# Optimization experiments

Measured on AMD Instinct MI355X. Metric: run time of the kernel, lower is better.

## Reference

```python
import jax, jax.numpy as jnp
import numpy as np

CURRENT_TIME = 1000.0
TIME_WEIGHT = 0.1
NEG_INF = -1e9


def setup_inputs() -> dict:
    key = jax.random.key(0)
    ks = jax.random.split(key, 7)
    B, M, D, C = 1024, 65536, 64, 16
    return {
        "query": jax.random.normal(ks[0], (B, D), dtype=jnp.float32),
        "context": jax.random.normal(ks[1], (B, C), dtype=jnp.float32),
        "mem_keys": jax.random.normal(ks[2], (M, D), dtype=jnp.float32) * 0.1,
        "mem_values": jax.random.normal(ks[3], (M, D), dtype=jnp.float32) * 0.1,
        "mem_contexts": jax.random.normal(ks[4], (M, C), dtype=jnp.float32) * 0.1,
        "mem_timestamps": jax.random.uniform(ks[5], (M, 1), dtype=jnp.float32) * CURRENT_TIME,
        "used_mask": jax.random.randint(ks[6], (M,), 0, 2) > 0,
    }


def reference(query, context, mem_keys, mem_values, mem_contexts, mem_timestamps, used_mask):
    # content score: [B, M]
    scores = jnp.einsum("bd,md->bm", query, mem_keys)
    # context score, scaled by 0.5
    scores = scores + 0.5 * jnp.einsum("bc,mc->bm", context, mem_contexts)
    # time-decay bias, scaled by 0.3 (broadcast over batch)
    decay = jnp.exp(-TIME_WEIGHT * (CURRENT_TIME - mem_timestamps[:, 0]))  # [M]
    scores = scores + 0.3 * decay[None, :]
    # unused slots get -1e9 exactly as torch.full init
    scores = jnp.where(used_mask[None, :], scores, NEG_INF)
    attn = jax.nn.softmax(scores, axis=-1)
    return jnp.einsum("bm,md->bd", attn, mem_values)
```

## Files before the change

kernel.cpp:

```cpp
#include <hip/hip_runtime.h>

typedef float f32x4 __attribute__((ext_vector_type(4)));
typedef __bf16 bf16x8 __attribute__((ext_vector_type(8)));
typedef unsigned int u32;
typedef unsigned short u16;

#define MTOT 65536
#define BTOT 1024
#define DD 64
#define LOG2E 1.44269504088896340736f
#define MFMA __builtin_amdgcn_mfma_f32_16x16x32_bf16

#define NROWBLK ((MTOT + BTOT) * 24 / 256)
#define NVTBLK  (MTOT / 64)
#define ESPACE  (DD * BTOT + BTOT)
#define NSLICE  8

__device__ __forceinline__ u16 f2bf(float f) { return __builtin_bit_cast(u16, (__bf16)f); }
__device__ __forceinline__ u32 pk2(float a, float b) {
    return (u32)f2bf(a) | ((u32)f2bf(b) << 16);
}
__device__ __forceinline__ bf16x8 ldg8(const u16* p) { return *reinterpret_cast<const bf16x8*>(p); }
__device__ __forceinline__ float fexp2(float x) {
#if __has_builtin(__builtin_amdgcn_exp2f)
    return __builtin_amdgcn_exp2f(x);
#else
    return exp2f(x);
#endif
}
__device__ __forceinline__ void glds16(const void* g, void* l) {
    __builtin_amdgcn_global_load_lds((const __attribute__((address_space(1))) u32*)g,
                                     (__attribute__((address_space(3))) u32*)l, 16, 0, 0);
}

__global__ __launch_bounds__(256)
void prep_all(const float* __restrict__ q, const float* __restrict__ ctx,
              const float* __restrict__ K, const float* __restrict__ CT,
              const float* __restrict__ TS, const int* __restrict__ mask,
              const float* __restrict__ V,
              u16* __restrict__ Qc, u16* __restrict__ KC, u16* __restrict__ Vt)
{
    __shared__ u16 L[64][68];
    const int blk = blockIdx.x, t = threadIdx.x;

    if (blk < NROWBLK) {
        const int R = MTOT + BTOT;
        int gid = blk * 256 + t;
        float4 v = {0.f, 0.f, 0.f, 0.f};
        u16* dst;
        if (gid < R * 16) {
            int row = gid >> 4, qd = gid & 15;
            bool isQ = row >= MTOT;
            int r2 = isQ ? row - MTOT : row;
            v = *reinterpret_cast<const float4*>((isQ ? q : K) + (size_t)r2 * 64 + qd * 4);
            if (isQ) { v.x *= LOG2E; v.y *= LOG2E; v.z *= LOG2E; v.w *= LOG2E; }
            dst = (isQ ? Qc : KC) + (size_t)r2 * 96 + qd * 4;
        } else if (gid < R * 20) {
            int i = gid - R * 16;
            int row = i >> 2, qd = i & 3;
            bool isQ = row >= MTOT;
            int r2 = isQ ? row - MTOT : row;
            v = *reinterpret_cast<const float4*>((isQ ? ctx : CT) + (size_t)r2 * 16 + qd * 4);
            if (isQ) { const float s = 0.5f * LOG2E; v.x *= s; v.y *= s; v.z *= s; v.w *= s; }
            dst = (isQ ? Qc : KC) + (size_t)r2 * 96 + 64 + qd * 4;
        } else {
            int i = gid - R * 20;
            int row = i >> 2, qd = i & 3;
            bool isQ = row >= MTOT;
            int r2 = isQ ? row - MTOT : row;
            if (qd == 0)
                v.x = isQ ? LOG2E
                          : (mask[r2] ? 0.3f * __expf(-0.1f * (1000.0f - TS[r2])) : -100.0f);
            dst = (isQ ? Qc : KC) + (size_t)r2 * 96 + 80 + qd * 4;
        }
        ushort4 o = { f2bf(v.x), f2bf(v.y), f2bf(v.z), f2bf(v.w) };
        *reinterpret_cast<ushort4*>(dst) = o;
        return;
    }

    const int m0 = (blk - NROWBLK) * 64;
#pragma unroll
    for (int p = 0; p < 4; ++p) {
        int fi = t + p * 256;
        int mi = fi >> 4, di = (fi & 15) << 2;
        float4 v = *reinterpret_cast<const float4*>(V + (size_t)(m0 + mi) * 64 + di);
        ushort4 o = { f2bf(v.x), f2bf(v.y), f2bf(v.z), f2bf(v.w) };
        *reinterpret_cast<ushort4*>(&L[mi][di]) = o;
    }
    __syncthreads();
    const int d = t >> 2, seg = t & 3;
    u32 pk[8];
#pragma unroll
    for (int pr = 0; pr < 8; ++pr) {
        int c0 = seg * 16 + pr * 2;
        int g32 = c0 >> 5;
        int i0 = c0 & 31, i1 = (c0 + 1) & 31;
        int mp0 = g32 * 32 + (i0 >> 1) + (i0 & 1) * 16;
        int mp1 = g32 * 32 + (i1 >> 1) + (i1 & 1) * 16;
        pk[pr] = (u32)L[mp0][d] | ((u32)L[mp1][d] << 16);
    }
    uint4 A = {pk[0], pk[1], pk[2], pk[3]}, B4 = {pk[4], pk[5], pk[6], pk[7]};
    u16* dst = Vt + (size_t)d * MTOT + m0 + seg * 16;
    *reinterpret_cast<uint4*>(dst)     = A;
    *reinterpret_cast<uint4*>(dst + 8) = B4;
}

__global__ __launch_bounds__(512, 4)
void epmem_mfma(const u16* __restrict__ Qc, const u16* __restrict__ KCg,
                const u16* __restrict__ Vtg,
                float* __restrict__ pl, float* __restrict__ pacc,
                int mper, int NB)
{
    __shared__ __align__(16) u16 KCs[2][64 * 96];
    __shared__ __align__(16) u16 Vts[2][64 * 64];
    __shared__ __align__(16) u16 Pb[8][32][40];

    const int tid = threadIdx.x;
    const int w = tid >> 6, lane = tid & 63;
    const int l15 = lane & 15, g = lane >> 4;

    const int bid = blockIdx.x;
    const int o = (bid & 7) * (NB >> 3) + (bid >> 3);
    const int rt = o & 3, ch = o >> 2;
    const int rbase = rt * 256 + w * 32;

    const u16* qp = Qc + (size_t)(rbase + l15) * 96 + g * 8;
    bf16x8 qf[2][3];
#pragma unroll
    for (int sb = 0; sb < 2; ++sb)
#pragma unroll
        for (int c = 0; c < 3; ++c)
            qf[sb][c] = ldg8(qp + sb * 16 * 96 + c * 32);

    const int m0 = ch * mper;
    const int m1 = (m0 + mper < MTOT) ? (m0 + mper) : MTOT;
    const int ntiles = (m1 > m0) ? ((m1 - m0) >> 6) : 0;

    int kgo[3], vgo[2];
    if (w < 4) {
#pragma unroll
        for (int i = 0; i < 3; ++i) {
            int ol = w * 3072 + i * 1024 + lane * 16;
            int row = ol / 192;
            int c = (ol - row * 192) >> 4;
            int u = (c < 8) ? (c ^ (row & 7)) : (8 + ((c & 3) ^ (row & 3)));
            kgo[i] = row * 192 + u * 16;
        }
#pragma unroll
        for (int i = 0; i < 2; ++i) {
            int ol = w * 2048 + i * 1024 + lane * 16;
            int row = ol >> 7, c = (ol >> 4) & 7;
            int u = c ^ (row & 7);
            vgo[i] = row * (MTOT * 2) + u * 16;
        }
    }

    const u32 ow = (l15 == 0) ? 0x3F803F80u : 0u;
    const uint4 ou = {ow, ow, ow, ow};
    const bf16x8 onesf = __builtin_bit_cast(bf16x8, ou);

    f32x4 acc[2][4];
    f32x4 accl[2];
#pragma unroll
    for (int sb = 0; sb < 2; ++sb) {
        accl[sb] = (f32x4){0, 0, 0, 0};
#pragma unroll
        for (int d4 = 0; d4 < 4; ++d4) acc[sb][d4] = (f32x4){0, 0, 0, 0};
    }

    if (ntiles > 0 && w < 4) {
        const char* kb = (const char*)KCg + (size_t)m0 * 192;
        const char* vb = (const char*)Vtg + (size_t)m0 * 2;
#pragma unroll
        for (int i = 0; i < 3; ++i) glds16(kb + kgo[i], (char*)KCs[0] + w * 3072 + i * 1024);
#pragma unroll
        for (int i = 0; i < 2; ++i) glds16(vb + vgo[i], (char*)Vts[0] + w * 2048 + i * 1024);
    }
    __syncthreads();

    char* pbw = (char*)Pb[w];
    const int xr = l15 & 7;
    const int x3 = l15 & 3;

    int cur = 0;
    for (int t = 0; t < ntiles; ++t) {
        if (t + 1 < ntiles && w < 4) {
            int mt = m0 + ((t + 1) << 6);
            const char* kb = (const char*)KCg + (size_t)mt * 192;
            const char* vb = (const char*)Vtg + (size_t)mt * 2;
            int nb = cur ^ 1;
#pragma unroll
            for (int i = 0; i < 3; ++i) glds16(kb + kgo[i], (char*)KCs[nb] + w * 3072 + i * 1024);
#pragma unroll
            for (int i = 0; i < 2; ++i) glds16(vb + vgo[i], (char*)Vts[nb] + w * 2048 + i * 1024);
        }
        const char* kcb = (const char*)KCs[cur];
        const char* vtb = (const char*)Vts[cur];

#pragma unroll
        for (int j = 0; j < 2; ++j) {
            bf16x8 kf[2][3];
#pragma unroll
            for (int s = 0; s < 2; ++s) {
                int row = j * 32 + s * 16 + l15;
                kf[s][0] = *reinterpret_cast<const bf16x8*>(kcb + row * 192 + (((0 + g) ^ xr) << 4));
                kf[s][1] = *reinterpret_cast<const bf16x8*>(kcb + row * 192 + (((4 + g) ^ xr) << 4));
                kf[s][2] = *reinterpret_cast<const bf16x8*>(kcb + row * 192 + ((8 + (g ^ x3)) << 4));
            }
            bf16x8 vf[4];
#pragma unroll
            for (int d4 = 0; d4 < 4; ++d4) {
                int row = d4 * 16 + l15;
                vf[d4] = *reinterpret_cast<const bf16x8*>(vtb + row * 128 + (((j * 4 + g) ^ xr) << 4));
            }

            f32x4 S00 = {0,0,0,0}, S01 = {0,0,0,0}, S10 = {0,0,0,0}, S11 = {0,0,0,0};
            S00 = MFMA(qf[0][0], kf[0][0], S00,0,0,0); S00 = MFMA(qf[0][1], kf[0][1], S00,0,0,0); S00 = MFMA(qf[0][2], kf[0][2], S00,0,0,0);
            S01 = MFMA(qf[0][0], kf[1][0], S01,0,0,0); S01 = MFMA(qf[0][1], kf[1][1], S01,0,0,0); S01 = MFMA(qf[0][2], kf[1][2], S01,0,0,0);
            S10 = MFMA(qf[1][0], kf[0][0], S10,0,0,0); S10 = MFMA(qf[1][1], kf[0][1], S10,0,0,0); S10 = MFMA(qf[1][2], kf[0][2], S10,0,0,0);
            S11 = MFMA(qf[1][0], kf[1][0], S11,0,0,0); S11 = MFMA(qf[1][1], kf[1][1], S11,0,0,0); S11 = MFMA(qf[1][2], kf[1][2], S11,0,0,0);

#pragma unroll
            for (int r = 0; r < 4; ++r) {
                float p00 = fexp2(S00[r]), p01 = fexp2(S01[r]);
                float p10 = fexp2(S10[r]), p11 = fexp2(S11[r]);
                int row0 = g * 4 + r, row1 = 16 + g * 4 + r;
                int cw = (((l15 >> 2) ^ r) << 4) | ((l15 & 3) << 2);
                *(u32*)(pbw + row0 * 80 + cw) = pk2(p00, p01);
                *(u32*)(pbw + row1 * 80 + cw) = pk2(p10, p11);
            }
            bf16x8 pa0 = *reinterpret_cast<const bf16x8*>(pbw + l15 * 80        + ((g ^ x3) << 4));
            bf16x8 pa1 = *reinterpret_cast<const bf16x8*>(pbw + (16 + l15) * 80 + ((g ^ x3) << 4));

            acc[0][0] = MFMA(pa0, vf[0], acc[0][0],0,0,0); acc[0][1] = MFMA(pa0, vf[1], acc[0][1],0,0,0);
            acc[0][2] = MFMA(pa0, vf[2], acc[0][2],0,0,0); acc[0][3] = MFMA(pa0, vf[3], acc[0][3],0,0,0);
            acc[1][0] = MFMA(pa1, vf[0], acc[1][0],0,0,0); acc[1][1] = MFMA(pa1, vf[1], acc[1][1],0,0,0);
            acc[1][2] = MFMA(pa1, vf[2], acc[1][2],0,0,0); acc[1][3] = MFMA(pa1, vf[3], acc[1][3],0,0,0);
            accl[0] = MFMA(pa0, onesf, accl[0],0,0,0);
            accl[1] = MFMA(pa1, onesf, accl[1],0,0,0);
        }
        __syncthreads();
        cur ^= 1;
    }

    if (l15 == 0) {
#pragma unroll
        for (int sb = 0; sb < 2; ++sb)
            *reinterpret_cast<f32x4*>(pl + (size_t)ch * BTOT + rbase + sb * 16 + g * 4) = accl[sb];
    }

    float* bp = pacc + ((size_t)ch * DD + l15) * BTOT + rbase + g * 4;
#pragma unroll
    for (int sb = 0; sb < 2; ++sb)
#pragma unroll
        for (int d4 = 0; d4 < 4; ++d4)
            *reinterpret_cast<f32x4*>(bp + (size_t)(d4 * 16) * BTOT + sb * 16) = acc[sb][d4];
}

__global__ __launch_bounds__(256)
void combineA(const float* __restrict__ pl, const float* __restrict__ pacc,
              float* __restrict__ part, int cper)
{
    int e = blockIdx.x * 256 + threadIdx.x;
    int s = blockIdx.y;
    int c0 = s * cper;
    float v0 = 0.f, v1 = 0.f;
    if (e < DD * BTOT) {
        const float* p = pacc + (size_t)c0 * (DD * BTOT) + e;
#pragma unroll 2
        for (int i = 0; i + 1 < cper; i += 2) {
            v0 += p[(size_t)i * (DD * BTOT)];
            v1 += p[(size_t)(i + 1) * (DD * BTOT)];
        }
        if (cper & 1) v0 += p[(size_t)(cper - 1) * (DD * BTOT)];
    } else {
        const float* p = pl + (size_t)c0 * BTOT + (e - DD * BTOT);
#pragma unroll 2
        for (int i = 0; i + 1 < cper; i += 2) {
            v0 += p[(size_t)i * BTOT];
            v1 += p[(size_t)(i + 1) * BTOT];
        }
        if (cper & 1) v0 += p[(size_t)(cper - 1) * BTOT];
    }
    part[(size_t)s * ESPACE + e] = v0 + v1;
}

__global__ __launch_bounds__(256)
void combineB(const float* __restrict__ part, float* __restrict__ out)
{
    int t = blockIdx.x * 256 + threadIdx.x;
    int d = t >> 10, b = t & 1023;
    float v = 0.f, lssum = 0.f;
#pragma unroll
    for (int s = 0; s < NSLICE; ++s) {
        v     += part[(size_t)s * ESPACE + t];
        lssum += part[(size_t)s * ESPACE + DD * BTOT + b];
    }
    out[(size_t)b * DD + d] = v / lssum;
}

extern "C" void kernel_launch(void* const* d_in, const int* in_sizes, int n_in,
                              void* d_out, int out_size, void* d_ws, size_t ws_size,
                              hipStream_t stream)
{
    const float* q    = (const float*)d_in[0];
    const float* ctx  = (const float*)d_in[1];
    const float* K    = (const float*)d_in[2];
    const float* V    = (const float*)d_in[3];
    const float* CT   = (const float*)d_in[4];
    const float* TS   = (const float*)d_in[5];
    const int*   mask = (const int*)d_in[6];

    char* wsb = (char*)d_ws;
    u16* Qc = (u16*)(wsb);
    u16* KC = (u16*)(wsb + 196608);
    u16* Vt = (u16*)(wsb + 196608 + 12582912);
    size_t fixed = 196608 + 12582912 + 8388608;

    size_t chunk = (size_t)BTOT * (DD + 1) * sizeof(float);
    size_t partB = (size_t)NSLICE * ESPACE * sizeof(float);
    int SPLIT = (int)((ws_size - fixed - partB) / chunk);
    if (SPLIT > 128) SPLIT = 128;
    SPLIT &= ~7;
    if (SPLIT < 8) SPLIT = 8;

    float* pl   = (float*)(wsb + fixed);
    float* pacc = pl + (size_t)SPLIT * BTOT;
    float* part = pacc + (size_t)SPLIT * DD * BTOT;

    int mper = ((MTOT + SPLIT - 1) / SPLIT + 63) & ~63;
    int cper = SPLIT / NSLICE;

    prep_all<<<NROWBLK + NVTBLK, 256, 0, stream>>>(q, ctx, K, CT, TS, mask, V, Qc, KC, Vt);

    int NB = 4 * SPLIT;
    epmem_mfma<<<NB, 512, 0, stream>>>(Qc, KC, Vt, pl, pacc, mper, NB);

    dim3 gA((ESPACE + 255) / 256, NSLICE);
    combineA<<<gA, 256, 0, stream>>>(pl, pacc, part, cper);
    combineB<<<(DD * BTOT) / 256, 256, 0, stream>>>(part, (float*)d_out);
}
```

Baseline: 55.55 us.

## Compact active memory slots so attention runs only over used entries

Adds count, scan and scatter kernels that build a compacted index list of the memory slots whose mask is set, along with their time-decay bias. The prep kernel then gathers keys, contexts and values through that index, and the MFMA attention kernel sizes its per-chunk range from the device-side active count. With a random half-empty mask this roughly halves the attention work. In exchange it adds three small launches, including a serial single-thread scan over 256 block counts, plus indirect gathers in prep.

Result: slower. 71.45 us (+28.6%).

```diff
diff --git a/kernel.cpp b/kernel.cpp
--- a/kernel.cpp
+++ b/kernel.cpp
@@ -34,14 +34,62 @@
 }
 
 __global__ __launch_bounds__(256)
+void k_count(const int* __restrict__ mask, int* __restrict__ blockCount)
+{
+    int t = threadIdx.x;
+    int m = blockIdx.x * 256 + t;
+    int active = mask[m] != 0;
+    unsigned long long bal = __ballot(active);
+    __shared__ int wc[4];
+    if ((t & 63) == 0) wc[t >> 6] = __popcll(bal);
+    __syncthreads();
+    if (t == 0) blockCount[blockIdx.x] = wc[0] + wc[1] + wc[2] + wc[3];
+}
+
+__global__ void k_scan(const int* __restrict__ blockCount, int* __restrict__ blockOff,
+                       int* __restrict__ MaPtr, int nb)
+{
+    if (threadIdx.x == 0 && blockIdx.x == 0) {
+        int s = 0;
+        for (int i = 0; i < nb; ++i) { blockOff[i] = s; s += blockCount[i]; }
+        *MaPtr = s;
+    }
+}
+
+__global__ __launch_bounds__(256)
+void k_scatter(const int* __restrict__ mask, const float* __restrict__ TS,
+               const int* __restrict__ blockOff,
+               int* __restrict__ idxc, float* __restrict__ biasc)
+{
+    int t = threadIdx.x;
+    int m = blockIdx.x * 256 + t;
+    int active = mask[m] != 0;
+    unsigned long long bal = __ballot(active);
+    int lane = t & 63, wid = t >> 6;
+    __shared__ int wc[4];
+    if (lane == 0) wc[wid] = __popcll(bal);
+    __syncthreads();
+    int base = blockOff[blockIdx.x];
+    for (int w = 0; w < wid; ++w) base += wc[w];
+    int rank = __popcll(bal & ((1ull << lane) - 1ull));
+    if (active) {
+        int dst = base + rank;
+        idxc[dst]  = m;
+        biasc[dst] = 0.3f * __expf(-0.1f * (1000.0f - TS[m]));
+    }
+}
+
+__global__ __launch_bounds__(256)
 void prep_all(const float* __restrict__ q, const float* __restrict__ ctx,
               const float* __restrict__ K, const float* __restrict__ CT,
-              const float* __restrict__ TS, const int* __restrict__ mask,
               const float* __restrict__ V,
+              const int* __restrict__ MaPtr, const int* __restrict__ idxc,
+              const float* __restrict__ biasc,
               u16* __restrict__ Qc, u16* __restrict__ KC, u16* __restrict__ Vt)
 {
     __shared__ u16 L[64][68];
     const int blk = blockIdx.x, t = threadIdx.x;
+    const int Ma = *MaPtr;
 
     if (blk < NROWBLK) {
         const int R = MTOT + BTOT;
@@ -51,27 +99,42 @@
         if (gid < R * 16) {
             int row = gid >> 4, qd = gid & 15;
             bool isQ = row >= MTOT;
-            int r2 = isQ ? row - MTOT : row;
-            v = *reinterpret_cast<const float4*>((isQ ? q : K) + (size_t)r2 * 64 + qd * 4);
-            if (isQ) { v.x *= LOG2E; v.y *= LOG2E; v.z *= LOG2E; v.w *= LOG2E; }
-            dst = (isQ ? Qc : KC) + (size_t)r2 * 96 + qd * 4;
+            if (isQ) {
+                int r2 = row - MTOT;
+                v = *reinterpret_cast<const float4*>(q + (size_t)r2 * 64 + qd * 4);
+                v.x *= LOG2E; v.y *= LOG2E; v.z *= LOG2E; v.w *= LOG2E;
+                dst = Qc + (size_t)r2 * 96 + qd * 4;
+            } else {
+                if (row < Ma)
+                    v = *reinterpret_cast<const float4*>(K + (size_t)idxc[row] * 64 + qd * 4);
+                dst = KC + (size_t)row * 96 + qd * 4;
+            }
         } else if (gid < R * 20) {
             int i = gid - R * 16;
             int row = i >> 2, qd = i & 3;
             bool isQ = row >= MTOT;
-            int r2 = isQ ? row - MTOT : row;
-            v = *reinterpret_cast<const float4*>((isQ ? ctx : CT) + (size_t)r2 * 16 + qd * 4);
-            if (isQ) { const float s = 0.5f * LOG2E; v.x *= s; v.y *= s; v.z *= s; v.w *= s; }
-            dst = (isQ ? Qc : KC) + (size_t)r2 * 96 + 64 + qd * 4;
+            if (isQ) {
+                int r2 = row - MTOT;
+                v = *reinterpret_cast<const float4*>(ctx + (size_t)r2 * 16 + qd * 4);
+                const float s = 0.5f * LOG2E; v.x *= s; v.y *= s; v.z *= s; v.w *= s;
+                dst = Qc + (size_t)r2 * 96 + 64 + qd * 4;
+            } else {
+                if (row < Ma)
+                    v = *reinterpret_cast<const float4*>(CT + (size_t)idxc[row] * 16 + qd * 4);
+                dst = KC + (size_t)row * 96 + 64 + qd * 4;
+            }
         } else {
             int i = gid - R * 20;
             int row = i >> 2, qd = i & 3;
             bool isQ = row >= MTOT;
-            int r2 = isQ ? row - MTOT : row;
-            if (qd == 0)
-                v.x = isQ ? LOG2E
-                          : (mask[r2] ? 0.3f * __expf(-0.1f * (1000.0f - TS[r2])) : -100.0f);
-            dst = (isQ ? Qc : KC) + (size_t)r2 * 96 + 80 + qd * 4;
+            if (isQ) {
+                int r2 = row - MTOT;
+                if (qd == 0) v.x = LOG2E;
+                dst = Qc + (size_t)r2 * 96 + 80 + qd * 4;
+            } else {
+                if (qd == 0) v.x = (row < Ma) ? biasc[row] : -1000.0f;
+                dst = KC + (size_t)row * 96 + 80 + qd * 4;
+            }
         }
         ushort4 o = { f2bf(v.x), f2bf(v.y), f2bf(v.z), f2bf(v.w) };
         *reinterpret_cast<ushort4*>(dst) = o;
@@ -83,7 +146,10 @@
     for (int p = 0; p < 4; ++p) {
         int fi = t + p * 256;
         int mi = fi >> 4, di = (fi & 15) << 2;
-        float4 v = *reinterpret_cast<const float4*>(V + (size_t)(m0 + mi) * 64 + di);
+        int r = m0 + mi;
+        float4 v = {0.f, 0.f, 0.f, 0.f};
+        if (r < Ma)
+            v = *reinterpret_cast<const float4*>(V + (size_t)idxc[r] * 64 + di);
         ushort4 o = { f2bf(v.x), f2bf(v.y), f2bf(v.z), f2bf(v.w) };
         *reinterpret_cast<ushort4*>(&L[mi][di]) = o;
     }
@@ -107,9 +173,9 @@
 
 __global__ __launch_bounds__(512, 4)
 void epmem_mfma(const u16* __restrict__ Qc, const u16* __restrict__ KCg,
-                const u16* __restrict__ Vtg,
+                const u16* __restrict__ Vtg, const int* __restrict__ MaPtr,
                 float* __restrict__ pl, float* __restrict__ pacc,
-                int mper, int NB)
+                int SPLIT, int NB)
 {
     __shared__ __align__(16) u16 KCs[2][64 * 96];
     __shared__ __align__(16) u16 Vts[2][64 * 64];
@@ -132,8 +198,11 @@
         for (int c = 0; c < 3; ++c)
             qf[sb][c] = ldg8(qp + sb * 16 * 96 + c * 32);
 
+    const int Ma = *MaPtr;
+    const int Mpad = (Ma + 63) & ~63;
+    const int mper = ((Mpad + SPLIT - 1) / SPLIT + 63) & ~63;
     const int m0 = ch * mper;
-    const int m1 = (m0 + mper < MTOT) ? (m0 + mper) : MTOT;
+    const int m1 = (m0 + mper < Mpad) ? (m0 + mper) : Mpad;
     const int ntiles = (m1 > m0) ? ((m1 - m0) >> 6) : 0;
 
     int kgo[3], vgo[2];
@@ -317,24 +386,35 @@
     u16* Vt = (u16*)(wsb + 196608 + 12582912);
     size_t fixed = 196608 + 12582912 + 8388608;
 
+    int*   MaPtr      = (int*)(wsb + fixed);
+    int*   blockCount = (int*)(wsb + fixed + 4096);
+    int*   blockOff   = (int*)(wsb + fixed + 8192);
+    int*   idxc       = (int*)(wsb + fixed + 12288);
+    float* biasc      = (float*)(wsb + fixed + 12288 + 262144);
+    size_t scratch_end = fixed + 12288 + 524288;
+
     size_t chunk = (size_t)BTOT * (DD + 1) * sizeof(float);
     size_t partB = (size_t)NSLICE * ESPACE * sizeof(float);
-    int SPLIT = (int)((ws_size - fixed - partB) / chunk);
+    int SPLIT = (int)((ws_size - scratch_end - partB) / chunk);
     if (SPLIT > 128) SPLIT = 128;
     SPLIT &= ~7;
     if (SPLIT < 8) SPLIT = 8;
 
-    float* pl   = (float*)(wsb + fixed);
+    float* pl   = (float*)(wsb + scratch_end);
     float* pacc = pl + (size_t)SPLIT * BTOT;
     float* part = pacc + (size_t)SPLIT * DD * BTOT;
 
-    int mper = ((MTOT + SPLIT - 1) / SPLIT + 63) & ~63;
     int cper = SPLIT / NSLICE;
 
-    prep_all<<<NROWBLK + NVTBLK, 256, 0, stream>>>(q, ctx, K, CT, TS, mask, V, Qc, KC, Vt);
+    k_count  <<<MTOT / 256, 256, 0, stream>>>(mask, blockCount);
+    k_scan   <<<1, 64, 0, stream>>>(blockCount, blockOff, MaPtr, MTOT / 256);
+    k_scatter<<<MTOT / 256, 256, 0, stream>>>(mask, TS, blockOff, idxc, biasc);
+
+    prep_all<<<NROWBLK + NVTBLK, 256, 0, stream>>>(q, ctx, K, CT, V, MaPtr, idxc, biasc,
+                                                   Qc, KC, Vt);
 
     int NB = 4 * SPLIT;
-    epmem_mfma<<<NB, 512, 0, stream>>>(Qc, KC, Vt, pl, pacc, mper, NB);
+    epmem_mfma<<<NB, 512, 0, stream>>>(Qc, KC, Vt, MaPtr, pl, pacc, SPLIT, NB);
 
     dim3 gA((ESPACE + 255) / 256, NSLICE);
     combineA<<<gA, 256, 0, stream>>>(pl, pacc, part, cper);
```
